# Kernel tuning notes

Hardware: AMD Instinct MI355X
Metric: run time of the kernel (lower is better)

The kernel has to match this reference:

```python
import jax, jax.numpy as jnp
import numpy as np

B, T, FIN, D = 8, 512, 256, 128


def setup_inputs() -> dict:
    key = jax.random.key(0)
    ks = jax.random.split(key, 12)
    s = lambda fan_in: 1.0 / np.sqrt(fan_in)
    return {
        "x": jax.random.normal(ks[0], (B, T, FIN), jnp.float32),
        "S0": jnp.zeros((B, 1, D, D), jnp.float32),
        "Z0": jnp.zeros((B, 1, D), jnp.float32),
        "gamma": jnp.ones((FIN,), jnp.float32),
        "beta": jnp.zeros((FIN,), jnp.float32),
        "Wk": jax.random.normal(ks[1], (FIN, D), jnp.float32) * s(FIN),
        "Wq": jax.random.normal(ks[2], (FIN, D), jnp.float32) * s(FIN),
        "Wv": jax.random.normal(ks[3], (FIN, D), jnp.float32) * s(FIN),
        "W1": jax.random.normal(ks[4], (D, D), jnp.float32) * s(D),
        "b1": jnp.zeros((D,), jnp.float32),
        "W2": jax.random.normal(ks[5], (D, D), jnp.float32) * s(D),
        "b2": jnp.zeros((D,), jnp.float32),
        "Ws": jax.random.normal(ks[6], (FIN, D), jnp.float32) * s(FIN),
        "bs": jnp.zeros((D,), jnp.float32),
    }


def reference(x, S0, Z0, gamma, beta, Wk, Wq, Wv, W1, b1, W2, b2, Ws, bs):
    CLAMP = 1e20
    # LayerNorm over feature dim
    mu = jnp.mean(x, axis=-1, keepdims=True)
    var = jnp.var(x, axis=-1, keepdims=True)
    xn = (x - mu) / jnp.sqrt(var + 1e-5) * gamma + beta
    # phi(x) = elu(x) + 1
    K = jax.nn.elu(xn @ Wk) + 1.0  # [B,T,D]
    Q = jax.nn.elu(xn @ Wq) + 1.0  # [B,T,D]
    V = xn @ Wv                     # [B,T,D]
    # outer-product state recurrence via cumsum (faithful to original)
    outer = jnp.einsum('bti,btj->btij', K, V)            # [B,T,D,D]
    S = jnp.clip(jnp.cumsum(outer, axis=1), -CLAMP, CLAMP) + S0  # [B,T,D,D]
    Z = jnp.clip(jnp.cumsum(K, axis=1), -CLAMP, CLAMP) + Z0      # [B,T,D]
    numerator = jnp.einsum('bti,btil->btl', Q, S)        # [B,T,D]
    denominator = jnp.einsum('bti,bti->bt', Q, Z)[..., None] + 1e-5
    out = numerator / denominator
    # FFN: relu(relu(out W1 + b1) W2 + b2)
    out = jax.nn.relu(jax.nn.relu(out @ W1 + b1) @ W2 + b2)
    # residual shortcut from normed input
    out = out + xn @ Ws + bs
    S_out = S.reshape(B, T, D * D)
    return out, S_out, Z
```

## Files before the change

kernel.cpp:

```cpp
#include <hip/hip_runtime.h>


constexpr int BB = 8, TT = 512, FIN_ = 256, DD = 128;
constexpr int NROW = BB * TT;
constexpr int CLEN = 64, NCH = 8;
constexpr float CLAMPV = 1e20f;

typedef float f4v __attribute__((ext_vector_type(4)));

__global__ __launch_bounds__(256) void ln_kernel(
    const float* __restrict__ x, const float* __restrict__ gamma,
    const float* __restrict__ beta, float* __restrict__ xn)
{
  int tid = threadIdx.x;
  int row = blockIdx.x * 4 + (tid >> 6);
  int lane = tid & 63;
  float4 v = *(const float4*)&x[row * FIN_ + lane * 4];
  float sum = v.x + v.y + v.z + v.w;
  float sq  = v.x * v.x + v.y * v.y + v.z * v.z + v.w * v.w;
#pragma unroll
  for (int off = 1; off < 64; off <<= 1) {
    sum += __shfl_xor(sum, off);
    sq  += __shfl_xor(sq, off);
  }
  float mu  = sum * (1.0f / FIN_);
  float var = sq * (1.0f / FIN_) - mu * mu;
  float rs  = rsqrtf(var + 1e-5f);
  float4 g = *(const float4*)&gamma[lane * 4];
  float4 b = *(const float4*)&beta[lane * 4];
  float4 o;
  o.x = (v.x - mu) * rs * g.x + b.x;
  o.y = (v.y - mu) * rs * g.y + b.y;
  o.z = (v.z - mu) * rs * g.z + b.z;
  o.w = (v.w - mu) * rs * g.w + b.w;
  *(float4*)&xn[row * FIN_ + lane * 4] = o;
}

__global__ __launch_bounds__(256) void gemm_qkvs(
    const float* __restrict__ xn,
    const float* __restrict__ Wk, const float* __restrict__ Wq,
    const float* __restrict__ Wv, const float* __restrict__ Ws,
    const float* __restrict__ bs,
    float* __restrict__ Kb, float* __restrict__ Qb,
    float* __restrict__ Vb, float* __restrict__ Rb)
{
  int ct = blockIdx.x, rt = blockIdx.y;
  int mat = ct >> 1, cb = (ct & 1) * 64;
  const float* W = (mat == 0) ? Wk : (mat == 1) ? Wq : (mat == 2) ? Wv : Ws;
  float* Ob      = (mat == 0) ? Kb : (mat == 1) ? Qb : (mat == 2) ? Vb : Rb;
  __shared__ float As[16][64];
  __shared__ float Bs[16][64];
  int tid = threadIdx.x;
  int tn = tid & 15, tm = tid >> 4;
  int lm = tid >> 2, lq = tid & 3;
  int lk = tid >> 4, ln4 = (tid & 15) * 4;
  float acc[4][4] = {};
  for (int k0 = 0; k0 < FIN_; k0 += 16) {
    float4 av = *(const float4*)&xn[(rt * 64 + lm) * FIN_ + k0 + lq * 4];
    As[lq * 4 + 0][lm] = av.x;
    As[lq * 4 + 1][lm] = av.y;
    As[lq * 4 + 2][lm] = av.z;
    As[lq * 4 + 3][lm] = av.w;
    *(float4*)&Bs[lk][ln4] = *(const float4*)&W[(k0 + lk) * DD + cb + ln4];
    __syncthreads();
#pragma unroll
    for (int k = 0; k < 16; k++) {
      float4 a = *(const float4*)&As[k][tm * 4];
      float4 b = *(const float4*)&Bs[k][tn * 4];
      float ar[4] = {a.x, a.y, a.z, a.w};
      float br[4] = {b.x, b.y, b.z, b.w};
#pragma unroll
      for (int i = 0; i < 4; i++)
#pragma unroll
        for (int j = 0; j < 4; j++) acc[i][j] += ar[i] * br[j];
    }
    __syncthreads();
  }
#pragma unroll
  for (int i = 0; i < 4; i++) {
    int row = rt * 64 + tm * 4 + i;
    int col = cb + tn * 4;
    float vals[4];
#pragma unroll
    for (int j = 0; j < 4; j++) {
      float v = acc[i][j];
      if (mat <= 1) v = (v > 0.f) ? v + 1.f : expf(v);
      else if (mat == 3) v += bs[col + j];
      vals[j] = v;
    }
    float4 o = make_float4(vals[0], vals[1], vals[2], vals[3]);
    *(float4*)&Ob[row * DD + col] = o;
  }
}

__global__ __launch_bounds__(256) void chunksum_kernel(
    const float* __restrict__ Kb, const float* __restrict__ Vb,
    float* __restrict__ chunkS, float* __restrict__ chunkz)
{
  int jt = blockIdx.x, c = blockIdx.y, b = blockIdx.z, tid = threadIdx.x;
  __shared__ float Ks[CLEN][DD];
  __shared__ float Vs[CLEN][32];
  const float* Kc = Kb + (b * TT + c * CLEN) * DD;
  const float* Vc = Vb + (b * TT + c * CLEN) * DD + jt * 32;
  for (int u = 0; u < 8; u++) {
    int idx = u * 256 + tid;
    int t = idx >> 5, c4 = (idx & 31) * 4;
    *(float4*)&Ks[t][c4] = *(const float4*)&Kc[t * DD + c4];
  }
  for (int u = 0; u < 2; u++) {
    int idx = u * 256 + tid;
    int t = idx >> 3, c4 = (idx & 7) * 4;
    *(float4*)&Vs[t][c4] = *(const float4*)&Vc[t * DD + c4];
  }
  __syncthreads();
  int ti = tid >> 3, tj = tid & 7;
  int i0 = ti * 4, jl = tj * 4;
  float acc[4][4] = {};
  for (int t = 0; t < CLEN; t++) {
    float4 kv = *(const float4*)&Ks[t][i0];
    float4 vv = *(const float4*)&Vs[t][jl];
    float kr[4] = {kv.x, kv.y, kv.z, kv.w};
    float vr[4] = {vv.x, vv.y, vv.z, vv.w};
#pragma unroll
    for (int i = 0; i < 4; i++)
#pragma unroll
      for (int j = 0; j < 4; j++) acc[i][j] += kr[i] * vr[j];
  }
  float* oS = chunkS + (b * NCH + c) * DD * DD + jt * 32;
#pragma unroll
  for (int i = 0; i < 4; i++)
    *(float4*)&oS[(i0 + i) * DD + jl] = *(float4*)&acc[i][0];
  if (jt == 0 && tid < DD) {
    float z = 0.f;
    for (int t = 0; t < CLEN; t++) z += Ks[t][tid];
    chunkz[(b * NCH + c) * DD + tid] = z;
  }
}

__global__ __launch_bounds__(256) void scan_kernel(
    const float* __restrict__ chunkS, const float* __restrict__ S0,
    float* __restrict__ prefS,
    const float* __restrict__ chunkz, const float* __restrict__ Z0,
    float* __restrict__ prefz)
{
  int b = blockIdx.y;
  if (blockIdx.x == 64) {
    int i = threadIdx.x;
    if (i < DD) {
      float z0v = Z0[b * DD + i];
      float acc = 0.f;
      for (int c = 0; c < NCH; c++) {
        prefz[(b * NCH + c) * DD + i] = acc + z0v;
        acc += chunkz[(b * NCH + c) * DD + i];
      }
    }
    return;
  }
  int idx = blockIdx.x * 256 + threadIdx.x;
  float s0v = S0[b * DD * DD + idx];
  float acc = 0.f;
  for (int c = 0; c < NCH; c++) {
    prefS[(b * NCH + c) * DD * DD + idx] = acc + s0v;
    acc += chunkS[(b * NCH + c) * DD * DD + idx];
  }
}

__global__ __launch_bounds__(256) void s_write_kernel(
    const float* __restrict__ Kb, const float* __restrict__ Vb,
    const float* __restrict__ prefS, float* __restrict__ Sout)
{
  int it = blockIdx.x, c = blockIdx.y, b = blockIdx.z;
  int i0 = it * 8;
  __shared__ float Vs[CLEN][DD];
  __shared__ float Ksm[CLEN][8];
  int tid = threadIdx.x;
  const float* Kc = Kb + (b * TT + c * CLEN) * DD;
  const float* Vc = Vb + (b * TT + c * CLEN) * DD;
  for (int u = 0; u < 8; u++) {
    int idx = u * 256 + tid;
    int t = idx >> 5, c4 = (idx & 31) * 4;
    *(float4*)&Vs[t][c4] = *(const float4*)&Vc[t * DD + c4];
  }
  for (int u = 0; u < 2; u++) {
    int idx = u * 256 + tid;
    int t = idx >> 3, r = idx & 7;
    Ksm[t][r] = Kc[t * DD + i0 + r];
  }
  __syncthreads();
  int irow = tid >> 5, jq = tid & 31;
  int j = jq * 4;
  float4 pref = *(const float4*)&prefS[(b * NCH + c) * DD * DD + (i0 + irow) * DD + j];
  float4 acc = make_float4(0.f, 0.f, 0.f, 0.f);
  float* So = Sout + (size_t)(b * TT + c * CLEN) * (DD * DD) + (i0 + irow) * DD + j;
#pragma unroll 4
  for (int t = 0; t < CLEN; t++) {
    float4 v4 = *(const float4*)&Vs[t][j];
    float kk = Ksm[t][irow];
    acc.x += kk * v4.x; acc.y += kk * v4.y;
    acc.z += kk * v4.z; acc.w += kk * v4.w;
    f4v o4;
    o4.x = fminf(fmaxf(pref.x + acc.x, -CLAMPV), CLAMPV);
    o4.y = fminf(fmaxf(pref.y + acc.y, -CLAMPV), CLAMPV);
    o4.z = fminf(fmaxf(pref.z + acc.z, -CLAMPV), CLAMPV);
    o4.w = fminf(fmaxf(pref.w + acc.w, -CLAMPV), CLAMPV);
    __builtin_nontemporal_store(o4, (f4v*)&So[(size_t)t * (DD * DD)]);
  }
}

__global__ __launch_bounds__(256) void attn_kernel(
    const float* __restrict__ Kb, const float* __restrict__ Qb,
    const float* __restrict__ Vb, const float* __restrict__ prefS,
    const float* __restrict__ prefz,
    float* __restrict__ Zout, float* __restrict__ attn_o)
{
  int sub = blockIdx.x, c = blockIdx.y, b = blockIdx.z, tid = threadIdx.x;
  int t0 = sub * 16;
  int tlim = t0 + 16;
  __shared__ float KsT[DD][CLEN + 1];
  __shared__ float Qs[16][DD + 1];
  __shared__ float sc[16][CLEN + 1];
  __shared__ float zeff[DD];
  __shared__ float den[16];
  const float* Kc = Kb + (b * TT + c * CLEN) * DD;
  const float* Qc = Qb + (b * TT + c * CLEN) * DD;
  const float* Vc = Vb + (b * TT + c * CLEN) * DD;
  for (int idx = tid; idx < tlim * 32; idx += 256) {
    int t = idx >> 5, c4 = (idx & 31) * 4;
    float4 v = *(const float4*)&Kc[t * DD + c4];
    KsT[c4 + 0][t] = v.x; KsT[c4 + 1][t] = v.y;
    KsT[c4 + 2][t] = v.z; KsT[c4 + 3][t] = v.w;
  }
  for (int idx = tid; idx < 16 * 32; idx += 256) {
    int r = idx >> 5, c4 = (idx & 31) * 4;
    float4 q = *(const float4*)&Qc[(t0 + r) * DD + c4];
    Qs[r][c4 + 0] = q.x; Qs[r][c4 + 1] = q.y;
    Qs[r][c4 + 2] = q.z; Qs[r][c4 + 3] = q.w;
  }
  if (tid < DD) zeff[tid] = prefz[(b * NCH + c) * DD + tid];
  __syncthreads();
  {
    int tm = tid >> 4, tn = tid & 15;
    if (tn * 4 < tlim) {
      float s0 = 0.f, s1 = 0.f, s2 = 0.f, s3 = 0.f;
#pragma unroll 4
      for (int k = 0; k < DD; k++) {
        float q = Qs[tm][k];
        s0 += q * KsT[k][tn * 4 + 0];
        s1 += q * KsT[k][tn * 4 + 1];
        s2 += q * KsT[k][tn * 4 + 2];
        s3 += q * KsT[k][tn * 4 + 3];
      }
      int t = t0 + tm;
      sc[tm][tn * 4 + 0] = (tn * 4 + 0 <= t) ? s0 : 0.f;
      sc[tm][tn * 4 + 1] = (tn * 4 + 1 <= t) ? s1 : 0.f;
      sc[tm][tn * 4 + 2] = (tn * 4 + 2 <= t) ? s2 : 0.f;
      sc[tm][tn * 4 + 3] = (tn * 4 + 3 <= t) ? s3 : 0.f;
    }
  }
  __syncthreads();
  if (tid < 16) {
    int t = t0 + tid;
    float d = 0.f;
    for (int tau = 0; tau <= t; tau++) d += sc[tid][tau];
    float dz = 0.f;
    for (int k = 0; k < DD; k++) dz += Qs[tid][k] * zeff[k];
    den[tid] = d + dz + 1e-5f;
  }
  __syncthreads();
  int tl = tid & 31, tg = tid >> 5;
  int l0 = tl * 4, r0 = tg * 2, r1 = tg * 2 + 1;
  float n0[4] = {}, n1[4] = {};
  for (int tau = 0; tau < tlim; tau++) {
    float4 v4 = *(const float4*)&Vc[tau * DD + l0];
    float sa = sc[r0][tau], sb = sc[r1][tau];
    n0[0] += sa * v4.x; n0[1] += sa * v4.y; n0[2] += sa * v4.z; n0[3] += sa * v4.w;
    n1[0] += sb * v4.x; n1[1] += sb * v4.y; n1[2] += sb * v4.z; n1[3] += sb * v4.w;
  }
  const float* P = prefS + (b * NCH + c) * DD * DD;
#pragma unroll 2
  for (int i = 0; i < DD; i++) {
    float4 p4 = *(const float4*)&P[i * DD + l0];
    float qa = Qs[r0][i], qb = Qs[r1][i];
    n0[0] += qa * p4.x; n0[1] += qa * p4.y; n0[2] += qa * p4.z; n0[3] += qa * p4.w;
    n1[0] += qb * p4.x; n1[1] += qb * p4.y; n1[2] += qb * p4.z; n1[3] += qb * p4.w;
  }
  float* og = attn_o + (size_t)(b * TT + c * CLEN + t0) * DD;
  {
    float da = den[r0], db = den[r1];
    float4 oa = make_float4(n0[0] / da, n0[1] / da, n0[2] / da, n0[3] / da);
    float4 ob = make_float4(n1[0] / db, n1[1] / db, n1[2] / db, n1[3] / db);
    *(float4*)&og[r0 * DD + l0] = oa;
    *(float4*)&og[r1 * DD + l0] = ob;
  }
  if (sub == 3 && tid < DD) {
    int i = tid;
    float a = zeff[i];
    for (int t = 0; t < CLEN; t++) {
      a += KsT[i][t];
      a = fminf(fmaxf(a, -CLAMPV), CLAMPV);
      __builtin_nontemporal_store(a, &Zout[(size_t)(b * TT + c * CLEN + t) * DD + i]);
    }
  }
}

__global__ __launch_bounds__(128) void ffn_kernel(
    const float* __restrict__ att, const float* __restrict__ res,
    const float* __restrict__ W1, const float* __restrict__ b1,
    const float* __restrict__ W2, const float* __restrict__ b2,
    float* __restrict__ outp)
{
  int rt = blockIdx.x, tid = threadIdx.x;
  __shared__ float As[16][129];
  __shared__ float H1[16][129];
  const float* ab = att + rt * 16 * DD;
  for (int u = 0; u < 4; u++) {
    int idx = u * 128 + tid;
    int r = idx >> 5, c4 = (idx & 31) * 4;
    float4 v = *(const float4*)&ab[r * DD + c4];
    As[r][c4 + 0] = v.x; As[r][c4 + 1] = v.y;
    As[r][c4 + 2] = v.z; As[r][c4 + 3] = v.w;
  }
  __syncthreads();
  int cn = tid & 31, rm = tid >> 5;
  int col = cn * 4, r0 = rm * 4;
  float acc[4][4] = {};
  for (int k = 0; k < DD; k++) {
    float4 w = *(const float4*)&W1[k * DD + col];
    float a[4];
#pragma unroll
    for (int i = 0; i < 4; i++) a[i] = As[r0 + i][k];
#pragma unroll
    for (int i = 0; i < 4; i++) {
      acc[i][0] += a[i] * w.x; acc[i][1] += a[i] * w.y;
      acc[i][2] += a[i] * w.z; acc[i][3] += a[i] * w.w;
    }
  }
  float4 bv = *(const float4*)&b1[col];
#pragma unroll
  for (int i = 0; i < 4; i++) {
    H1[r0 + i][col + 0] = fmaxf(acc[i][0] + bv.x, 0.f);
    H1[r0 + i][col + 1] = fmaxf(acc[i][1] + bv.y, 0.f);
    H1[r0 + i][col + 2] = fmaxf(acc[i][2] + bv.z, 0.f);
    H1[r0 + i][col + 3] = fmaxf(acc[i][3] + bv.w, 0.f);
  }
  __syncthreads();
  float acc2[4][4] = {};
  for (int k = 0; k < DD; k++) {
    float4 w = *(const float4*)&W2[k * DD + col];
    float a[4];
#pragma unroll
    for (int i = 0; i < 4; i++) a[i] = H1[r0 + i][k];
#pragma unroll
    for (int i = 0; i < 4; i++) {
      acc2[i][0] += a[i] * w.x; acc2[i][1] += a[i] * w.y;
      acc2[i][2] += a[i] * w.z; acc2[i][3] += a[i] * w.w;
    }
  }
  float4 b2v = *(const float4*)&b2[col];
#pragma unroll
  for (int i = 0; i < 4; i++) {
    int row = rt * 16 + r0 + i;
    float4 rv = *(const float4*)&res[row * DD + col];
    float4 o;
    o.x = fmaxf(acc2[i][0] + b2v.x, 0.f) + rv.x;
    o.y = fmaxf(acc2[i][1] + b2v.y, 0.f) + rv.y;
    o.z = fmaxf(acc2[i][2] + b2v.z, 0.f) + rv.z;
    o.w = fmaxf(acc2[i][3] + b2v.w, 0.f) + rv.w;
    *(float4*)&outp[row * DD + col] = o;
  }
}

extern "C" void kernel_launch(void* const* d_in, const int* in_sizes, int n_in,
                              void* d_out, int out_size, void* d_ws, size_t ws_size,
                              hipStream_t stream)
{
  const float* x     = (const float*)d_in[0];
  const float* S0    = (const float*)d_in[1];
  const float* Z0    = (const float*)d_in[2];
  const float* gamma = (const float*)d_in[3];
  const float* beta  = (const float*)d_in[4];
  const float* Wk    = (const float*)d_in[5];
  const float* Wq    = (const float*)d_in[6];
  const float* Wv    = (const float*)d_in[7];
  const float* W1    = (const float*)d_in[8];
  const float* b1    = (const float*)d_in[9];
  const float* W2    = (const float*)d_in[10];
  const float* b2    = (const float*)d_in[11];
  const float* Ws    = (const float*)d_in[12];
  const float* bs    = (const float*)d_in[13];

  float* out_main = (float*)d_out;
  float* Sout = out_main + NROW * DD;
  float* Zout = Sout + (size_t)NROW * DD * DD;

  float* ws_f   = (float*)d_ws;
  float* xn     = ws_f;
  float* Kb     = xn + 1048576;
  float* Qb     = Kb + 524288;
  float* Vb     = Qb + 524288;
  float* Rb     = Vb + 524288;
  float* chunkS = Rb + 524288;
  float* prefS  = chunkS + 1048576;
  float* chunkz = prefS + 1048576;
  float* prefz  = chunkz + 8192;
  float* attn_o = prefz + 8192;

  ln_kernel<<<NROW / 4, 256, 0, stream>>>(x, gamma, beta, xn);
  gemm_qkvs<<<dim3(8, 64), 256, 0, stream>>>(xn, Wk, Wq, Wv, Ws, bs, Kb, Qb, Vb, Rb);
  chunksum_kernel<<<dim3(4, NCH, BB), 256, 0, stream>>>(Kb, Vb, chunkS, chunkz);
  scan_kernel<<<dim3(65, BB), 256, 0, stream>>>(chunkS, S0, prefS, chunkz, Z0, prefz);
  s_write_kernel<<<dim3(16, NCH, BB), 256, 0, stream>>>(Kb, Vb, prefS, Sout);
  attn_kernel<<<dim3(4, NCH, BB), 256, 0, stream>>>(Kb, Qb, Vb, prefS, prefz, Zout, attn_o);
  ffn_kernel<<<NROW / 16, 128, 0, stream>>>(attn_o, Rb, W1, b1, W2, b2, out_main);
}
```

Measured before the change: 413.6 us.

## Fuse LayerNorm into GEMM, merge chunk-sum and scan, retune attention/FFN/S-write

LayerNorm statistics are computed inside the QKV GEMM blocks, and normalization is applied on the fly, removing the separate LN kernel and the xn buffer. The chunk-sum and scan kernels are merged into one prefix kernel that loops over chunks and writes prefix states directly. The attention kernel uses smaller query sub-tiles for more blocks, the FFN uses 256 threads, and the S write kernel uses 512-thread blocks and launches last. The aim is fewer launches and less intermediate memory traffic, at the cost of redundant LN statistics per column tile and a serial per-chunk loop in the prefix kernel.

New measurement: 402.2 us. -2.8%, faster.

```diff
diff --git a/kernel.cpp b/kernel.cpp
--- a/kernel.cpp
+++ b/kernel.cpp
@@ -8,36 +8,9 @@
 
 typedef float f4v __attribute__((ext_vector_type(4)));
 
-__global__ __launch_bounds__(256) void ln_kernel(
-    const float* __restrict__ x, const float* __restrict__ gamma,
-    const float* __restrict__ beta, float* __restrict__ xn)
-{
-  int tid = threadIdx.x;
-  int row = blockIdx.x * 4 + (tid >> 6);
-  int lane = tid & 63;
-  float4 v = *(const float4*)&x[row * FIN_ + lane * 4];
-  float sum = v.x + v.y + v.z + v.w;
-  float sq  = v.x * v.x + v.y * v.y + v.z * v.z + v.w * v.w;
-#pragma unroll
-  for (int off = 1; off < 64; off <<= 1) {
-    sum += __shfl_xor(sum, off);
-    sq  += __shfl_xor(sq, off);
-  }
-  float mu  = sum * (1.0f / FIN_);
-  float var = sq * (1.0f / FIN_) - mu * mu;
-  float rs  = rsqrtf(var + 1e-5f);
-  float4 g = *(const float4*)&gamma[lane * 4];
-  float4 b = *(const float4*)&beta[lane * 4];
-  float4 o;
-  o.x = (v.x - mu) * rs * g.x + b.x;
-  o.y = (v.y - mu) * rs * g.y + b.y;
-  o.z = (v.z - mu) * rs * g.z + b.z;
-  o.w = (v.w - mu) * rs * g.w + b.w;
-  *(float4*)&xn[row * FIN_ + lane * 4] = o;
-}
-
 __global__ __launch_bounds__(256) void gemm_qkvs(
-    const float* __restrict__ xn,
+    const float* __restrict__ x,
+    const float* __restrict__ gamma, const float* __restrict__ beta,
     const float* __restrict__ Wk, const float* __restrict__ Wq,
     const float* __restrict__ Wv, const float* __restrict__ Ws,
     const float* __restrict__ bs,
@@ -50,17 +23,41 @@
   float* Ob      = (mat == 0) ? Kb : (mat == 1) ? Qb : (mat == 2) ? Vb : Rb;
   __shared__ float As[16][64];
   __shared__ float Bs[16][64];
+  __shared__ float mu_s[64], rs_s[64];
   int tid = threadIdx.x;
+  {
+    int row = tid >> 2, q = tid & 3;
+    const float* xr = &x[(rt * 64 + row) * FIN_ + q * 64];
+    float sum = 0.f, sq = 0.f;
+#pragma unroll
+    for (int u = 0; u < 16; u++) {
+      float4 v = *(const float4*)&xr[u * 4];
+      sum += v.x + v.y + v.z + v.w;
+      sq  += v.x * v.x + v.y * v.y + v.z * v.z + v.w * v.w;
+    }
+    sum += __shfl_xor(sum, 1); sq += __shfl_xor(sq, 1);
+    sum += __shfl_xor(sum, 2); sq += __shfl_xor(sq, 2);
+    if (q == 0) {
+      float mu = sum * (1.0f / FIN_);
+      float var = sq * (1.0f / FIN_) - mu * mu;
+      mu_s[row] = mu;
+      rs_s[row] = rsqrtf(var + 1e-5f);
+    }
+  }
+  __syncthreads();
   int tn = tid & 15, tm = tid >> 4;
   int lm = tid >> 2, lq = tid & 3;
   int lk = tid >> 4, ln4 = (tid & 15) * 4;
   float acc[4][4] = {};
+  float mu = mu_s[lm], rs = rs_s[lm];
   for (int k0 = 0; k0 < FIN_; k0 += 16) {
-    float4 av = *(const float4*)&xn[(rt * 64 + lm) * FIN_ + k0 + lq * 4];
-    As[lq * 4 + 0][lm] = av.x;
-    As[lq * 4 + 1][lm] = av.y;
-    As[lq * 4 + 2][lm] = av.z;
-    As[lq * 4 + 3][lm] = av.w;
+    float4 av = *(const float4*)&x[(rt * 64 + lm) * FIN_ + k0 + lq * 4];
+    float4 g  = *(const float4*)&gamma[k0 + lq * 4];
+    float4 be = *(const float4*)&beta[k0 + lq * 4];
+    As[lq * 4 + 0][lm] = (av.x - mu) * rs * g.x + be.x;
+    As[lq * 4 + 1][lm] = (av.y - mu) * rs * g.y + be.y;
+    As[lq * 4 + 2][lm] = (av.z - mu) * rs * g.z + be.z;
+    As[lq * 4 + 3][lm] = (av.w - mu) * rs * g.w + be.w;
     *(float4*)&Bs[lk][ln4] = *(const float4*)&W[(k0 + lk) * DD + cb + ln4];
     __syncthreads();
 #pragma unroll
@@ -93,103 +90,236 @@
   }
 }
 
-__global__ __launch_bounds__(256) void chunksum_kernel(
+__global__ __launch_bounds__(256) void prefix_kernel(
     const float* __restrict__ Kb, const float* __restrict__ Vb,
-    float* __restrict__ chunkS, float* __restrict__ chunkz)
-{
-  int jt = blockIdx.x, c = blockIdx.y, b = blockIdx.z, tid = threadIdx.x;
-  __shared__ float Ks[CLEN][DD];
+    const float* __restrict__ S0, const float* __restrict__ Z0,
+    float* __restrict__ prefS, float* __restrict__ prefz)
+{
+  int jt = blockIdx.x, it = blockIdx.y, b = blockIdx.z;
+  int i0 = it * 16, j0 = jt * 32;
+  __shared__ float Ks[CLEN][16];
   __shared__ float Vs[CLEN][32];
+  int tid = threadIdx.x;
+  int il = tid >> 4, jl = tid & 15;
+  float2 s0v = *(const float2*)&S0[b * DD * DD + (i0 + il) * DD + j0 + jl * 2];
+  float acc0 = 0.f, acc1 = 0.f;
+  float zacc = 0.f;
+  float z0v = (jt == 0 && tid < 16) ? Z0[b * DD + i0 + tid] : 0.f;
+  for (int c = 0; c < NCH; c++) {
+    const float* Kc = Kb + (b * TT + c * CLEN) * DD;
+    const float* Vc = Vb + (b * TT + c * CLEN) * DD;
+    {
+      int t = tid >> 2, i4 = (tid & 3) * 4;
+      *(float4*)&Ks[t][i4] = *(const float4*)&Kc[t * DD + i0 + i4];
+    }
+#pragma unroll
+    for (int u = 0; u < 2; u++) {
+      int idx = u * 256 + tid;
+      int t = idx >> 3, j4 = (idx & 7) * 4;
+      *(float4*)&Vs[t][j4] = *(const float4*)&Vc[t * DD + j0 + j4];
+    }
+    __syncthreads();
+    float2 op = make_float2(acc0 + s0v.x, acc1 + s0v.y);
+    *(float2*)&prefS[(size_t)(b * NCH + c) * DD * DD + (i0 + il) * DD + j0 + jl * 2] = op;
+    if (jt == 0 && tid < 16)
+      prefz[(b * NCH + c) * DD + i0 + tid] = zacc + z0v;
+#pragma unroll 8
+    for (int t = 0; t < CLEN; t++) {
+      float k = Ks[t][il];
+      float2 v2 = *(const float2*)&Vs[t][jl * 2];
+      acc0 += k * v2.x;
+      acc1 += k * v2.y;
+    }
+    if (jt == 0 && tid < 16) {
+      float z = 0.f;
+#pragma unroll 8
+      for (int t = 0; t < CLEN; t++) z += Ks[t][tid];
+      zacc += z;
+    }
+    __syncthreads();
+  }
+}
+
+__global__ __launch_bounds__(256) void attn_kernel(
+    const float* __restrict__ Kb, const float* __restrict__ Qb,
+    const float* __restrict__ Vb, const float* __restrict__ prefS,
+    const float* __restrict__ prefz,
+    float* __restrict__ Zout, float* __restrict__ attn_o)
+{
+  int sub = blockIdx.x, c = blockIdx.y, b = blockIdx.z, tid = threadIdx.x;
+  int t0 = sub * 8;
+  int tlim = t0 + 8;
+  __shared__ float KsT[DD][CLEN + 2];
+  __shared__ float Qs[8][132];
+  __shared__ float sc[8][CLEN + 2];
+  __shared__ float zeff[DD];
+  __shared__ float den[8];
   const float* Kc = Kb + (b * TT + c * CLEN) * DD;
-  const float* Vc = Vb + (b * TT + c * CLEN) * DD + jt * 32;
-  for (int u = 0; u < 8; u++) {
-    int idx = u * 256 + tid;
+  const float* Qc = Qb + (b * TT + c * CLEN) * DD;
+  const float* Vc = Vb + (b * TT + c * CLEN) * DD;
+  for (int idx = tid; idx < tlim * 32; idx += 256) {
     int t = idx >> 5, c4 = (idx & 31) * 4;
-    *(float4*)&Ks[t][c4] = *(const float4*)&Kc[t * DD + c4];
-  }
-  for (int u = 0; u < 2; u++) {
-    int idx = u * 256 + tid;
-    int t = idx >> 3, c4 = (idx & 7) * 4;
-    *(float4*)&Vs[t][c4] = *(const float4*)&Vc[t * DD + c4];
-  }
-  __syncthreads();
-  int ti = tid >> 3, tj = tid & 7;
-  int i0 = ti * 4, jl = tj * 4;
-  float acc[4][4] = {};
-  for (int t = 0; t < CLEN; t++) {
-    float4 kv = *(const float4*)&Ks[t][i0];
-    float4 vv = *(const float4*)&Vs[t][jl];
-    float kr[4] = {kv.x, kv.y, kv.z, kv.w};
-    float vr[4] = {vv.x, vv.y, vv.z, vv.w};
-#pragma unroll
-    for (int i = 0; i < 4; i++)
-#pragma unroll
-      for (int j = 0; j < 4; j++) acc[i][j] += kr[i] * vr[j];
-  }
-  float* oS = chunkS + (b * NCH + c) * DD * DD + jt * 32;
-#pragma unroll
-  for (int i = 0; i < 4; i++)
-    *(float4*)&oS[(i0 + i) * DD + jl] = *(float4*)&acc[i][0];
-  if (jt == 0 && tid < DD) {
-    float z = 0.f;
-    for (int t = 0; t < CLEN; t++) z += Ks[t][tid];
-    chunkz[(b * NCH + c) * DD + tid] = z;
-  }
-}
-
-__global__ __launch_bounds__(256) void scan_kernel(
-    const float* __restrict__ chunkS, const float* __restrict__ S0,
-    float* __restrict__ prefS,
-    const float* __restrict__ chunkz, const float* __restrict__ Z0,
-    float* __restrict__ prefz)
-{
-  int b = blockIdx.y;
-  if (blockIdx.x == 64) {
-    int i = threadIdx.x;
-    if (i < DD) {
-      float z0v = Z0[b * DD + i];
-      float acc = 0.f;
-      for (int c = 0; c < NCH; c++) {
-        prefz[(b * NCH + c) * DD + i] = acc + z0v;
-        acc += chunkz[(b * NCH + c) * DD + i];
+    float4 v = *(const float4*)&Kc[t * DD + c4];
+    KsT[c4 + 0][t] = v.x; KsT[c4 + 1][t] = v.y;
+    KsT[c4 + 2][t] = v.z; KsT[c4 + 3][t] = v.w;
+  }
+  {
+    int r = tid >> 5, c4 = (tid & 31) * 4;
+    float4 q = *(const float4*)&Qc[(t0 + r) * DD + c4];
+    *(float4*)&Qs[r][c4] = q;
+  }
+  if (tid < DD) zeff[tid] = prefz[(b * NCH + c) * DD + tid];
+  __syncthreads();
+  {
+    int tm = tid >> 5, tn = tid & 31;
+    int tau0 = tn * 2;
+    if (tau0 < tlim) {
+      float s0 = 0.f, s1 = 0.f;
+#pragma unroll 8
+      for (int k = 0; k < DD; k++) {
+        float q = Qs[tm][k];
+        float2 kk = *(const float2*)&KsT[k][tau0];
+        s0 += q * kk.x;
+        s1 += q * kk.y;
       }
-    }
-    return;
-  }
-  int idx = blockIdx.x * 256 + threadIdx.x;
-  float s0v = S0[b * DD * DD + idx];
-  float acc = 0.f;
-  for (int c = 0; c < NCH; c++) {
-    prefS[(b * NCH + c) * DD * DD + idx] = acc + s0v;
-    acc += chunkS[(b * NCH + c) * DD * DD + idx];
-  }
-}
-
-__global__ __launch_bounds__(256) void s_write_kernel(
+      int t = t0 + tm;
+      sc[tm][tau0]     = (tau0     <= t) ? s0 : 0.f;
+      sc[tm][tau0 + 1] = (tau0 + 1 <= t) ? s1 : 0.f;
+    }
+  }
+  __syncthreads();
+  if (tid < 8) {
+    int t = t0 + tid;
+    float d = 0.f;
+    for (int tau = 0; tau <= t; tau++) d += sc[tid][tau];
+    float dz = 0.f;
+#pragma unroll 8
+    for (int k = 0; k < DD; k++) dz += Qs[tid][k] * zeff[k];
+    den[tid] = d + dz + 1e-5f;
+  }
+  __syncthreads();
+  int tl = tid & 31, r = tid >> 5;
+  int l0 = tl * 4;
+  float n0[4] = {};
+#pragma unroll 4
+  for (int tau = 0; tau < tlim; tau++) {
+    float4 v4 = *(const float4*)&Vc[tau * DD + l0];
+    float s = sc[r][tau];
+    n0[0] += s * v4.x; n0[1] += s * v4.y; n0[2] += s * v4.z; n0[3] += s * v4.w;
+  }
+  const float* P = prefS + (size_t)(b * NCH + c) * DD * DD;
+#pragma unroll 4
+  for (int i = 0; i < DD; i++) {
+    float4 p4 = *(const float4*)&P[i * DD + l0];
+    float q = Qs[r][i];
+    n0[0] += q * p4.x; n0[1] += q * p4.y; n0[2] += q * p4.z; n0[3] += q * p4.w;
+  }
+  float* og = attn_o + (size_t)(b * TT + c * CLEN + t0) * DD;
+  {
+    float dd = den[r];
+    float4 o = make_float4(n0[0] / dd, n0[1] / dd, n0[2] / dd, n0[3] / dd);
+    *(float4*)&og[r * DD + l0] = o;
+  }
+  if (sub == 7 && tid < DD) {
+    int i = tid;
+    float a = zeff[i];
+    for (int t = 0; t < CLEN; t++) {
+      a += KsT[i][t];
+      a = fminf(fmaxf(a, -CLAMPV), CLAMPV);
+      __builtin_nontemporal_store(a, &Zout[(size_t)(b * TT + c * CLEN + t) * DD + i]);
+    }
+  }
+}
+
+__global__ __launch_bounds__(256) void ffn_kernel(
+    const float* __restrict__ att, const float* __restrict__ res,
+    const float* __restrict__ W1, const float* __restrict__ b1,
+    const float* __restrict__ W2, const float* __restrict__ b2,
+    float* __restrict__ outp)
+{
+  int rt = blockIdx.x, tid = threadIdx.x;
+  __shared__ float As[16][132];
+  __shared__ float H1[16][132];
+  const float* ab = att + rt * 16 * DD;
+  {
+    int idx = tid;
+#pragma unroll
+    for (int u = 0; u < 2; u++, idx += 256) {
+      int r = idx >> 5, c4 = (idx & 31) * 4;
+      *(float4*)&As[r][c4] = *(const float4*)&ab[r * DD + c4];
+    }
+  }
+  __syncthreads();
+  int cn = tid & 31, rm = tid >> 5;
+  int col = cn * 4, r0 = rm * 2;
+  float acc[2][4] = {};
+#pragma unroll 8
+  for (int k = 0; k < DD; k++) {
+    float4 w = *(const float4*)&W1[k * DD + col];
+    float a0 = As[r0][k], a1 = As[r0 + 1][k];
+    acc[0][0] += a0 * w.x; acc[0][1] += a0 * w.y; acc[0][2] += a0 * w.z; acc[0][3] += a0 * w.w;
+    acc[1][0] += a1 * w.x; acc[1][1] += a1 * w.y; acc[1][2] += a1 * w.z; acc[1][3] += a1 * w.w;
+  }
+  float4 bv = *(const float4*)&b1[col];
+#pragma unroll
+  for (int i = 0; i < 2; i++) {
+    float4 h;
+    h.x = fmaxf(acc[i][0] + bv.x, 0.f);
+    h.y = fmaxf(acc[i][1] + bv.y, 0.f);
+    h.z = fmaxf(acc[i][2] + bv.z, 0.f);
+    h.w = fmaxf(acc[i][3] + bv.w, 0.f);
+    *(float4*)&H1[r0 + i][col] = h;
+  }
+  __syncthreads();
+  float acc2[2][4] = {};
+#pragma unroll 8
+  for (int k = 0; k < DD; k++) {
+    float4 w = *(const float4*)&W2[k * DD + col];
+    float a0 = H1[r0][k], a1 = H1[r0 + 1][k];
+    acc2[0][0] += a0 * w.x; acc2[0][1] += a0 * w.y; acc2[0][2] += a0 * w.z; acc2[0][3] += a0 * w.w;
+    acc2[1][0] += a1 * w.x; acc2[1][1] += a1 * w.y; acc2[1][2] += a1 * w.z; acc2[1][3] += a1 * w.w;
+  }
+  float4 b2v = *(const float4*)&b2[col];
+#pragma unroll
+  for (int i = 0; i < 2; i++) {
+    int row = rt * 16 + r0 + i;
+    float4 rv = *(const float4*)&res[row * DD + col];
+    float4 o;
+    o.x = fmaxf(acc2[i][0] + b2v.x, 0.f) + rv.x;
+    o.y = fmaxf(acc2[i][1] + b2v.y, 0.f) + rv.y;
+    o.z = fmaxf(acc2[i][2] + b2v.z, 0.f) + rv.z;
+    o.w = fmaxf(acc2[i][3] + b2v.w, 0.f) + rv.w;
+    *(float4*)&outp[row * DD + col] = o;
+  }
+}
+
+__global__ __launch_bounds__(512) void s_write_kernel(
     const float* __restrict__ Kb, const float* __restrict__ Vb,
     const float* __restrict__ prefS, float* __restrict__ Sout)
 {
   int it = blockIdx.x, c = blockIdx.y, b = blockIdx.z;
-  int i0 = it * 8;
+  int i0 = it * 16;
   __shared__ float Vs[CLEN][DD];
-  __shared__ float Ksm[CLEN][8];
+  __shared__ float Ksm[CLEN][16];
   int tid = threadIdx.x;
   const float* Kc = Kb + (b * TT + c * CLEN) * DD;
   const float* Vc = Vb + (b * TT + c * CLEN) * DD;
-  for (int u = 0; u < 8; u++) {
-    int idx = u * 256 + tid;
+#pragma unroll
+  for (int u = 0; u < 4; u++) {
+    int idx = u * 512 + tid;
     int t = idx >> 5, c4 = (idx & 31) * 4;
     *(float4*)&Vs[t][c4] = *(const float4*)&Vc[t * DD + c4];
   }
+#pragma unroll
   for (int u = 0; u < 2; u++) {
-    int idx = u * 256 + tid;
-    int t = idx >> 3, r = idx & 7;
+    int idx = u * 512 + tid;
+    int t = idx >> 4, r = idx & 15;
     Ksm[t][r] = Kc[t * DD + i0 + r];
   }
   __syncthreads();
   int irow = tid >> 5, jq = tid & 31;
   int j = jq * 4;
-  float4 pref = *(const float4*)&prefS[(b * NCH + c) * DD * DD + (i0 + irow) * DD + j];
+  float4 pref = *(const float4*)&prefS[(size_t)(b * NCH + c) * DD * DD + (i0 + irow) * DD + j];
   float4 acc = make_float4(0.f, 0.f, 0.f, 0.f);
   float* So = Sout + (size_t)(b * TT + c * CLEN) * (DD * DD) + (i0 + irow) * DD + j;
 #pragma unroll 4
@@ -207,169 +337,6 @@
   }
 }
 
-__global__ __launch_bounds__(256) void attn_kernel(
-    const float* __restrict__ Kb, const float* __restrict__ Qb,
-    const float* __restrict__ Vb, const float* __restrict__ prefS,
-    const float* __restrict__ prefz,
-    float* __restrict__ Zout, float* __restrict__ attn_o)
-{
-  int sub = blockIdx.x, c = blockIdx.y, b = blockIdx.z, tid = threadIdx.x;
-  int t0 = sub * 16;
-  int tlim = t0 + 16;
-  __shared__ float KsT[DD][CLEN + 1];
-  __shared__ float Qs[16][DD + 1];
-  __shared__ float sc[16][CLEN + 1];
-  __shared__ float zeff[DD];
-  __shared__ float den[16];
-  const float* Kc = Kb + (b * TT + c * CLEN) * DD;
-  const float* Qc = Qb + (b * TT + c * CLEN) * DD;
-  const float* Vc = Vb + (b * TT + c * CLEN) * DD;
-  for (int idx = tid; idx < tlim * 32; idx += 256) {
-    int t = idx >> 5, c4 = (idx & 31) * 4;
-    float4 v = *(const float4*)&Kc[t * DD + c4];
-    KsT[c4 + 0][t] = v.x; KsT[c4 + 1][t] = v.y;
-    KsT[c4 + 2][t] = v.z; KsT[c4 + 3][t] = v.w;
-  }
-  for (int idx = tid; idx < 16 * 32; idx += 256) {
-    int r = idx >> 5, c4 = (idx & 31) * 4;
-    float4 q = *(const float4*)&Qc[(t0 + r) * DD + c4];
-    Qs[r][c4 + 0] = q.x; Qs[r][c4 + 1] = q.y;
-    Qs[r][c4 + 2] = q.z; Qs[r][c4 + 3] = q.w;
-  }
-  if (tid < DD) zeff[tid] = prefz[(b * NCH + c) * DD + tid];
-  __syncthreads();
-  {
-    int tm = tid >> 4, tn = tid & 15;
-    if (tn * 4 < tlim) {
-      float s0 = 0.f, s1 = 0.f, s2 = 0.f, s3 = 0.f;
-#pragma unroll 4
-      for (int k = 0; k < DD; k++) {
-        float q = Qs[tm][k];
-        s0 += q * KsT[k][tn * 4 + 0];
-        s1 += q * KsT[k][tn * 4 + 1];
-        s2 += q * KsT[k][tn * 4 + 2];
-        s3 += q * KsT[k][tn * 4 + 3];
-      }
-      int t = t0 + tm;
-      sc[tm][tn * 4 + 0] = (tn * 4 + 0 <= t) ? s0 : 0.f;
-      sc[tm][tn * 4 + 1] = (tn * 4 + 1 <= t) ? s1 : 0.f;
-      sc[tm][tn * 4 + 2] = (tn * 4 + 2 <= t) ? s2 : 0.f;
-      sc[tm][tn * 4 + 3] = (tn * 4 + 3 <= t) ? s3 : 0.f;
-    }
-  }
-  __syncthreads();
-  if (tid < 16) {
-    int t = t0 + tid;
-    float d = 0.f;
-    for (int tau = 0; tau <= t; tau++) d += sc[tid][tau];
-    float dz = 0.f;
-    for (int k = 0; k < DD; k++) dz += Qs[tid][k] * zeff[k];
-    den[tid] = d + dz + 1e-5f;
-  }
-  __syncthreads();
-  int tl = tid & 31, tg = tid >> 5;
-  int l0 = tl * 4, r0 = tg * 2, r1 = tg * 2 + 1;
-  float n0[4] = {}, n1[4] = {};
-  for (int tau = 0; tau < tlim; tau++) {
-    float4 v4 = *(const float4*)&Vc[tau * DD + l0];
-    float sa = sc[r0][tau], sb = sc[r1][tau];
-    n0[0] += sa * v4.x; n0[1] += sa * v4.y; n0[2] += sa * v4.z; n0[3] += sa * v4.w;
-    n1[0] += sb * v4.x; n1[1] += sb * v4.y; n1[2] += sb * v4.z; n1[3] += sb * v4.w;
-  }
-  const float* P = prefS + (b * NCH + c) * DD * DD;
-#pragma unroll 2
-  for (int i = 0; i < DD; i++) {
-    float4 p4 = *(const float4*)&P[i * DD + l0];
-    float qa = Qs[r0][i], qb = Qs[r1][i];
-    n0[0] += qa * p4.x; n0[1] += qa * p4.y; n0[2] += qa * p4.z; n0[3] += qa * p4.w;
-    n1[0] += qb * p4.x; n1[1] += qb * p4.y; n1[2] += qb * p4.z; n1[3] += qb * p4.w;
-  }
-  float* og = attn_o + (size_t)(b * TT + c * CLEN + t0) * DD;
-  {
-    float da = den[r0], db = den[r1];
-    float4 oa = make_float4(n0[0] / da, n0[1] / da, n0[2] / da, n0[3] / da);
-    float4 ob = make_float4(n1[0] / db, n1[1] / db, n1[2] / db, n1[3] / db);
-    *(float4*)&og[r0 * DD + l0] = oa;
-    *(float4*)&og[r1 * DD + l0] = ob;
-  }
-  if (sub == 3 && tid < DD) {
-    int i = tid;
-    float a = zeff[i];
-    for (int t = 0; t < CLEN; t++) {
-      a += KsT[i][t];
-      a = fminf(fmaxf(a, -CLAMPV), CLAMPV);
-      __builtin_nontemporal_store(a, &Zout[(size_t)(b * TT + c * CLEN + t) * DD + i]);
-    }
-  }
-}
-
-__global__ __launch_bounds__(128) void ffn_kernel(
-    const float* __restrict__ att, const float* __restrict__ res,
-    const float* __restrict__ W1, const float* __restrict__ b1,
-    const float* __restrict__ W2, const float* __restrict__ b2,
-    float* __restrict__ outp)
-{
-  int rt = blockIdx.x, tid = threadIdx.x;
-  __shared__ float As[16][129];
-  __shared__ float H1[16][129];
-  const float* ab = att + rt * 16 * DD;
-  for (int u = 0; u < 4; u++) {
-    int idx = u * 128 + tid;
-    int r = idx >> 5, c4 = (idx & 31) * 4;
-    float4 v = *(const float4*)&ab[r * DD + c4];
-    As[r][c4 + 0] = v.x; As[r][c4 + 1] = v.y;
-    As[r][c4 + 2] = v.z; As[r][c4 + 3] = v.w;
-  }
-  __syncthreads();
-  int cn = tid & 31, rm = tid >> 5;
-  int col = cn * 4, r0 = rm * 4;
-  float acc[4][4] = {};
-  for (int k = 0; k < DD; k++) {
-    float4 w = *(const float4*)&W1[k * DD + col];
-    float a[4];
-#pragma unroll
-    for (int i = 0; i < 4; i++) a[i] = As[r0 + i][k];
-#pragma unroll
-    for (int i = 0; i < 4; i++) {
-      acc[i][0] += a[i] * w.x; acc[i][1] += a[i] * w.y;
-      acc[i][2] += a[i] * w.z; acc[i][3] += a[i] * w.w;
-    }
-  }
-  float4 bv = *(const float4*)&b1[col];
-#pragma unroll
-  for (int i = 0; i < 4; i++) {
-    H1[r0 + i][col + 0] = fmaxf(acc[i][0] + bv.x, 0.f);
-    H1[r0 + i][col + 1] = fmaxf(acc[i][1] + bv.y, 0.f);
-    H1[r0 + i][col + 2] = fmaxf(acc[i][2] + bv.z, 0.f);
-    H1[r0 + i][col + 3] = fmaxf(acc[i][3] + bv.w, 0.f);
-  }
-  __syncthreads();
-  float acc2[4][4] = {};
-  for (int k = 0; k < DD; k++) {
-    float4 w = *(const float4*)&W2[k * DD + col];
-    float a[4];
-#pragma unroll
-    for (int i = 0; i < 4; i++) a[i] = H1[r0 + i][k];
-#pragma unroll
-    for (int i = 0; i < 4; i++) {
-      acc2[i][0] += a[i] * w.x; acc2[i][1] += a[i] * w.y;
-      acc2[i][2] += a[i] * w.z; acc2[i][3] += a[i] * w.w;
-    }
-  }
-  float4 b2v = *(const float4*)&b2[col];
-#pragma unroll
-  for (int i = 0; i < 4; i++) {
-    int row = rt * 16 + r0 + i;
-    float4 rv = *(const float4*)&res[row * DD + col];
-    float4 o;
-    o.x = fmaxf(acc2[i][0] + b2v.x, 0.f) + rv.x;
-    o.y = fmaxf(acc2[i][1] + b2v.y, 0.f) + rv.y;
-    o.z = fmaxf(acc2[i][2] + b2v.z, 0.f) + rv.z;
-    o.w = fmaxf(acc2[i][3] + b2v.w, 0.f) + rv.w;
-    *(float4*)&outp[row * DD + col] = o;
-  }
-}
-
 extern "C" void kernel_launch(void* const* d_in, const int* in_sizes, int n_in,
                               void* d_out, int out_size, void* d_ws, size_t ws_size,
                               hipStream_t stream)
@@ -394,22 +361,18 @@
   float* Zout = Sout + (size_t)NROW * DD * DD;
 
   float* ws_f   = (float*)d_ws;
-  float* xn     = ws_f;
-  float* Kb     = xn + 1048576;
+  float* Kb     = ws_f;
   float* Qb     = Kb + 524288;
   float* Vb     = Qb + 524288;
   float* Rb     = Vb + 524288;
-  float* chunkS = Rb + 524288;
-  float* prefS  = chunkS + 1048576;
-  float* chunkz = prefS + 1048576;
-  float* prefz  = chunkz + 8192;
+  float* prefS  = Rb + 524288;
+  float* prefz  = prefS + 1048576;
   float* attn_o = prefz + 8192;
 
-  ln_kernel<<<NROW / 4, 256, 0, stream>>>(x, gamma, beta, xn);
-  gemm_qkvs<<<dim3(8, 64), 256, 0, stream>>>(xn, Wk, Wq, Wv, Ws, bs, Kb, Qb, Vb, Rb);
-  chunksum_kernel<<<dim3(4, NCH, BB), 256, 0, stream>>>(Kb, Vb, chunkS, chunkz);
-  scan_kernel<<<dim3(65, BB), 256, 0, stream>>>(chunkS, S0, prefS, chunkz, Z0, prefz);
-  s_write_kernel<<<dim3(16, NCH, BB), 256, 0, stream>>>(Kb, Vb, prefS, Sout);
-  attn_kernel<<<dim3(4, NCH, BB), 256, 0, stream>>>(Kb, Qb, Vb, prefS, prefz, Zout, attn_o);
-  ffn_kernel<<<NROW / 16, 128, 0, stream>>>(attn_o, Rb, W1, b1, W2, b2, out_main);
-}
+  gemm_qkvs<<<dim3(8, 64), 256, 0, stream>>>(x, gamma, beta, Wk, Wq, Wv, Ws, bs,
+                                             Kb, Qb, Vb, Rb);
+  prefix_kernel<<<dim3(4, 8, BB), 256, 0, stream>>>(Kb, Vb, S0, Z0, prefS, prefz);
+  attn_kernel<<<dim3(8, NCH, BB), 256, 0, stream>>>(Kb, Qb, Vb, prefS, prefz, Zout, attn_o);
+  ffn_kernel<<<NROW / 16, 256, 0, stream>>>(attn_o, Rb, W1, b1, W2, b2, out_main);
+  s_write_kernel<<<dim3(8, NCH, BB), 512, 0, stream>>>(Kb, Vb, prefS, Sout);
+}
```
